# Kernel tuning notes

Hardware: AMD Instinct MI355X
Metric: run time of the kernel (lower is better)

## Reference

```python
import jax, jax.numpy as jnp
import numpy as np

B, P, S = 128, 10, 8
L, BF = 81, 75
OF, MF2 = 40, 20
C = 64
H = 3 * C  # hidden_size = 192
NCHAR = 8
EPS = 1e-5


def setup_inputs() -> dict:
    key = jax.random.key(0)
    ks = jax.random.split(key, 24)
    n = lambda i, shp: jax.random.normal(ks[i], shp, jnp.float32)
    w = lambda i, shp: jax.random.normal(ks[i], shp, jnp.float32) * 0.02
    return {
        "board": n(0, (B, P, S, L, BF)),
        "order": n(1, (B, P, S, OF)),
        "message": n(2, (B, P, S, MF2)),
        "other_ind": jax.random.uniform(ks[3], (B, P, 7), jnp.float32),
        "me_ind": jax.random.uniform(ks[4], (B, P, 7), jnp.float32),
        "h0": n(5, (P, B, H)),
        "c0": n(6, (P, B, H)),
        "Wb1": w(7, (1024, L * BF)), "bb1": jnp.zeros((1024,), jnp.float32),
        "Wb2": w(8, (256, 1024)), "bb2": jnp.zeros((256,), jnp.float32),
        "Wb3": w(9, (C, 256)), "bb3": jnp.zeros((C,), jnp.float32),
        "Wo1": w(10, (128, OF)), "bo1": jnp.zeros((128,), jnp.float32),
        "Wo2": w(11, (32, 128)), "bo2": jnp.zeros((32,), jnp.float32),
        "Wo3": w(12, (C, 32)), "bo3": jnp.zeros((C,), jnp.float32),
        "Wm1": w(13, (64, MF2)), "bm1": jnp.zeros((64,), jnp.float32),
        "Wm2": w(14, (32, 64)), "bm2": jnp.zeros((32,), jnp.float32),
        "Wm3": w(15, (C, 32)), "bm3": jnp.zeros((C,), jnp.float32),
        "g1": jnp.ones((C,), jnp.float32), "be1": jnp.zeros((C,), jnp.float32),
        "g2": jnp.ones((C,), jnp.float32), "be2": jnp.zeros((C,), jnp.float32),
        "g3": jnp.ones((C,), jnp.float32), "be3": jnp.zeros((C,), jnp.float32),
        "Wih": w(16, (4 * H, H)), "Whh": w(17, (4 * H, H)),
        "bih": jnp.zeros((4 * H,), jnp.float32), "bhh": jnp.zeros((4 * H,), jnp.float32),
        "Wf1": w(18, (256, S * H)), "bf1": jnp.zeros((256,), jnp.float32),
        "Wf2": w(19, (NCHAR, 256 + 14)), "bf2": jnp.zeros((NCHAR,), jnp.float32),
    }


def _mlp3(x, W1, b1, W2, b2, W3, b3):
    x = jax.nn.relu(x @ W1.T + b1)
    x = jax.nn.relu(x @ W2.T + b2)
    return x @ W3.T + b3


def _bn_relu(x, g, b):
    # x: [b, C, S]; BatchNorm1d in training mode -> biased batch stats over (N, L)
    m = x.mean(axis=(0, 2), keepdims=True)
    v = jnp.mean((x - m) ** 2, axis=(0, 2), keepdims=True)
    return jax.nn.relu(g[None, :, None] * (x - m) * jax.lax.rsqrt(v + EPS) + b[None, :, None])


def _forward(board, order, message, other_ind, me_ind, h0, c0,
             Wb1, bb1, Wb2, bb2, Wb3, bb3, Wo1, bo1, Wo2, bo2, Wo3, bo3,
             Wm1, bm1, Wm2, bm2, Wm3, bm3, g1, be1, g2, be2, g3, be3,
             Wih, Whh, bih, bhh, Wf1, bf1, Wf2, bf2):
    num_step = board.shape[2]

    def per_past(board_p, order_p, msg_p, oi_p, mi_p, h, c):
        bb = board_p.shape[0]
        bf = _mlp3(board_p.reshape(bb * num_step, -1), Wb1, bb1, Wb2, bb2, Wb3, bb3)
        bf = _bn_relu(jnp.swapaxes(bf.reshape(bb, num_step, -1), 1, 2), g1, be1)
        of = _mlp3(order_p.reshape(bb * num_step, -1), Wo1, bo1, Wo2, bo2, Wo3, bo3)
        of = _bn_relu(jnp.swapaxes(of.reshape(bb, num_step, -1), 1, 2), g2, be2)
        mf = _mlp3(msg_p.reshape(bb * num_step, -1), Wm1, bm1, Wm2, bm2, Wm3, bm3)
        mf = _bn_relu(jnp.swapaxes(mf.reshape(bb, num_step, -1), 1, 2), g3, be3)
        x_feat = jnp.concatenate([bf, of, mf], axis=-1)              # [b, C, 3S]
        x_feat = jnp.transpose(jnp.swapaxes(x_feat, 1, 2), (2, 0, 1))  # [C, b, 3S]
        x_feat = x_feat.reshape(num_step, bb, -1)                    # [S, b, H] (same C-order reindex as torch)

        def step(carry, xt):
            h_, c_ = carry
            gates = xt @ Wih.T + bih + h_ @ Whh.T + bhh
            i, f, g_, o = jnp.split(gates, 4, axis=-1)
            c_ = jax.nn.sigmoid(f) * c_ + jax.nn.sigmoid(i) * jnp.tanh(g_)
            h_ = jax.nn.sigmoid(o) * jnp.tanh(c_)
            return (h_, c_), h_

        _, outs = jax.lax.scan(step, (h, c), x_feat)  # [S, b, H]
        x = jnp.swapaxes(outs, 0, 1).reshape(bb, -1)  # [b, S*H]
        x = jax.nn.relu(x @ Wf1.T + bf1)
        x = jnp.concatenate([x, oi_p, mi_p], axis=-1)  # [b, 256+14]
        return x @ Wf2.T + bf2

    per = jax.vmap(per_past)(
        jnp.swapaxes(board, 0, 1), jnp.swapaxes(order, 0, 1), jnp.swapaxes(message, 0, 1),
        jnp.swapaxes(other_ind, 0, 1), jnp.swapaxes(me_ind, 0, 1), h0, c0)  # [P, b, NCHAR]
    return per.sum(axis=0)


def reference(board, order, message, other_ind, me_ind, h0, c0,
              Wb1, bb1, Wb2, bb2, Wb3, bb3, Wo1, bo1, Wo2, bo2, Wo3, bo3,
              Wm1, bm1, Wm2, bm2, Wm3, bm3, g1, be1, g2, be2, g3, be3,
              Wih, Whh, bih, bhh, Wf1, bf1, Wf2, bf2):
    return _forward(board, order, message, other_ind, me_ind, h0, c0,
                    Wb1, bb1, Wb2, bb2, Wb3, bb3, Wo1, bo1, Wo2, bo2, Wo3, bo3,
                    Wm1, bm1, Wm2, bm2, Wm3, bm3, g1, be1, g2, be2, g3, be3,
                    Wih, Whh, bih, bhh, Wf1, bf1, Wf2, bf2)
```

## Files before the change

### kernel.cpp

```cpp
#include <hip/hip_runtime.h>
#include <stdint.h>

typedef unsigned short u16;
typedef __bf16 v8bf __attribute__((ext_vector_type(8)));
typedef float  v4f  __attribute__((ext_vector_type(4)));

__device__ __forceinline__ u16 f2bf(float f) {
    union { float f; unsigned u; } x; x.f = f;
    unsigned r = (x.u + 0x7FFFu + ((x.u >> 16) & 1u)) >> 16;
    return (u16)r;
}
__device__ __forceinline__ float sigf(float x) { return 1.f / (1.f + __expf(-x)); }
__device__ __forceinline__ void gload(const u16* src, u16* ldst) {
    __builtin_amdgcn_global_load_lds((const __attribute__((address_space(1))) void*)src,
                                     (__attribute__((address_space(3))) void*)ldst, 16, 0, 0);
}

#define OFF_ABF    0UL
#define OFF_XINBF  0UL
#define OFF_XG     3932160UL
#define OFF_FC1    44728320UL
#define OFF_WB1    125829120UL
#define OFF_C1     138412032UL
#define OFF_WB2    159383552UL
#define OFF_WB3    165150720UL
#define OFF_BFE    165216256UL
#define OFF_OFE    167837696UL
#define OFF_MFE    170459136UL
#define OFF_WIH    173095936UL
#define OFF_WHH    173390848UL
#define OFF_WF1    173685760UL
#define OFF_BSUM   174472192UL

__global__ void __launch_bounds__(256) conv_board(const float* __restrict__ src, u16* __restrict__ dst)
{
    int bid = blockIdx.x;
    int row = bid / 6, chunk = bid - row * 6;
    int k0 = chunk * 1024 + threadIdx.x * 4;
    const float* s = src + (long)row * 6075 + k0;
    u16* d = dst + (long)row * 6144 + k0;
    if (k0 + 4 <= 6075) {
        float f0 = s[0], f1 = s[1], f2 = s[2], f3 = s[3];
        uint2 v;
        v.x = (unsigned)f2bf(f0) | ((unsigned)f2bf(f1) << 16);
        v.y = (unsigned)f2bf(f2) | ((unsigned)f2bf(f3) << 16);
        *(uint2*)d = v;
    } else {
#pragma unroll
        for (int z = 0; z < 4; ++z) {
            int k = k0 + z;
            d[z] = f2bf(k < 6075 ? s[z] : 0.f);
        }
    }
}

__global__ void __launch_bounds__(256) conv_weights(
    const float* __restrict__ Wb1, const float* __restrict__ Wb2, const float* __restrict__ Wb3,
    const float* __restrict__ Wih, const float* __restrict__ Whh, const float* __restrict__ Wf1,
    const float* __restrict__ bih, const float* __restrict__ bhh,
    u16* __restrict__ dWb1, u16* __restrict__ dWb2, u16* __restrict__ dWb3,
    u16* __restrict__ dWih, u16* __restrict__ dWhh, u16* __restrict__ dWf1,
    float* __restrict__ bsum)
{
    const long C0 = 6291456, C1 = 6553600, C2 = 6586368, C3 = 6733824,
               C4 = 6881280, C5 = 7274496, C6 = 7275264;
    for (long i = (long)blockIdx.x * 256 + threadIdx.x; i < C6; i += (long)gridDim.x * 256) {
        if (i < C0) {
            int r = (int)(i / 6144), k = (int)(i % 6144);
            dWb1[i] = f2bf(k < 6075 ? Wb1[(long)r * 6075 + k] : 0.f);
        } else if (i < C1) {
            long j = i - C0;
            dWb2[j] = f2bf(Wb2[j]);
        } else if (i < C2) {
            long j = i - C1;
            dWb3[j] = f2bf(j < 16384 ? Wb3[j] : 0.f);
        } else if (i < C3) {
            long j = i - C2;
            dWih[j] = f2bf(Wih[j]);
        } else if (i < C4) {
            long j = i - C3;
            dWhh[j] = f2bf(Whh[j]);
        } else if (i < C5) {
            long j = i - C4;
            dWf1[j] = f2bf(Wf1[j]);
        } else {
            long j = i - C5;
            bsum[j] = bih[j] + bhh[j];
        }
    }
}

#define G160_LDS 73728
__global__ void __launch_bounds__(256, 2)
gemm160(const u16* __restrict__ A, const u16* __restrict__ B,
        const float* __restrict__ bias, u16* __restrict__ C, int K)
{
    extern __shared__ __align__(16) u16 smem[];
    const int tid = threadIdx.x, wv = tid >> 6, lane = tid & 63;
    const int bid = blockIdx.x;
    const int k8 = bid & 7;
    const int j  = bid >> 3;
    const int rowt = k8 + (j >> 3) * 8;
    const int col  = j & 7;
    const long m0 = (long)rowt * 160;
    const long n0 = (long)col * 128;

    const int sr8 = lane >> 3;
    const int sslot = (lane & 7) ^ sr8;
    const u16* Ag = A + (m0 + wv * 8 + sr8) * (long)K + sslot * 8;
    const u16* Bg = B + (n0 + wv * 8 + sr8) * (long)K + sslot * 8;
    const int wr = wv >> 1, wc = wv & 1;
    const int wm = wr * 80, wn = wc * 64;
    const int fr = lane & 15, hi = lane >> 4, fx = fr & 7;

    const int nk = K >> 6;
    v4f acc[5][4] = {};

    auto STAGE = [&](int buf, int t) {
        const long k0 = (long)t * 64;
        const int ab = buf * 18432;
#pragma unroll
        for (int r = 0; r < 5; ++r)
            gload(Ag + (long)r * 32 * K + k0, smem + ab + r * 2048 + wv * 512);
#pragma unroll
        for (int r = 0; r < 4; ++r)
            gload(Bg + (long)r * 32 * K + k0, smem + ab + 10240 + r * 2048 + wv * 512);
    };
    auto LDA_ = [&](int buf, int ks, int i) -> v8bf {
        return *(const v8bf*)(smem + buf * 18432 + (wm + i * 16 + fr) * 64 + ((ks * 4 + hi) ^ fx) * 8);
    };
    auto LDB_ = [&](int buf, int ks, int j2) -> v8bf {
        return *(const v8bf*)(smem + buf * 18432 + 10240 + (wn + j2 * 16 + fr) * 64 + ((ks * 4 + hi) ^ fx) * 8);
    };

    STAGE(0, 0);
    STAGE(1, 1);
    for (int t = 0; t < nk; ++t) {
        const int buf = t & 1;
        if (t + 1 < nk) { asm volatile("s_waitcnt vmcnt(9)" ::: "memory"); }
        else            { asm volatile("s_waitcnt vmcnt(0)" ::: "memory"); }
        asm volatile("s_barrier" ::: "memory");
        __builtin_amdgcn_s_setprio(1);
        v8bf a0[5], a1[5], b0[4], b1[4];
#pragma unroll
        for (int j2 = 0; j2 < 4; ++j2) b0[j2] = LDB_(buf, 0, j2);
#pragma unroll
        for (int i = 0; i < 5; ++i) a0[i] = LDA_(buf, 0, i);
        __builtin_amdgcn_sched_barrier(0);
#pragma unroll
        for (int j2 = 0; j2 < 4; ++j2) b1[j2] = LDB_(buf, 1, j2);
#pragma unroll
        for (int i = 0; i < 5; ++i) a1[i] = LDA_(buf, 1, i);
#pragma unroll
        for (int i = 0; i < 5; ++i)
#pragma unroll
            for (int j2 = 0; j2 < 4; ++j2)
                acc[i][j2] = __builtin_amdgcn_mfma_f32_16x16x32_bf16(a0[i], b0[j2], acc[i][j2], 0, 0, 0);
        __builtin_amdgcn_sched_barrier(0);
        __builtin_amdgcn_s_setprio(0);
        asm volatile("s_waitcnt lgkmcnt(0)" ::: "memory");
        __builtin_amdgcn_sched_barrier(0);
        asm volatile("s_barrier" ::: "memory");
        if (t + 2 < nk) STAGE(buf, t + 2);
        __builtin_amdgcn_s_setprio(1);
#pragma unroll
        for (int i = 0; i < 5; ++i)
#pragma unroll
            for (int j2 = 0; j2 < 4; ++j2)
                acc[i][j2] = __builtin_amdgcn_mfma_f32_16x16x32_bf16(a1[i], b1[j2], acc[i][j2], 0, 0, 0);
        __builtin_amdgcn_s_setprio(0);
    }

#pragma unroll
    for (int i = 0; i < 5; ++i) {
        const long mr = m0 + wm + i * 16 + hi * 4;
#pragma unroll
        for (int j2 = 0; j2 < 4; ++j2) {
            const long n = n0 + wn + j2 * 16 + fr;
            float bv = bias[n];
#pragma unroll
            for (int r = 0; r < 4; ++r) {
                float v = fmaxf(acc[i][j2][r] + bv, 0.f);
                C[(mr + r) * 1024L + n] = f2bf(v);
            }
        }
    }
}

#define L23_LDS 81920
__global__ void __launch_bounds__(512, 1)
gemm_l23(const u16* __restrict__ A, const u16* __restrict__ B, const float* __restrict__ b2,
         const u16* __restrict__ W3, const float* __restrict__ b3, float* __restrict__ Out)
{
    extern __shared__ __align__(16) u16 smem[];
    const int tid = threadIdx.x, wv = tid >> 6, lane = tid & 63;
    const long m0 = (long)blockIdx.x * 64;
    const int sr8 = lane >> 3;
    const int sslot = (lane & 7) ^ sr8;
    const u16* Ag = A + (m0 + wv * 8 + sr8) * 1024L + sslot * 8;
    const u16* Bg = B + (wv * 8 + sr8) * 1024L + sslot * 8;
    const int wr = wv >> 2, wc = wv & 3;
    const int wm = wr * 32, wn = wc * 64;
    const int fr = lane & 15, hi = lane >> 4, fx = fr & 7;

    v4f acc[2][4] = {};

    auto STAGE = [&](int buf, int t) {
        const long k0 = (long)t * 64;
        const int ab = buf * 20480;
        gload(Ag + k0, smem + ab + wv * 512);
#pragma unroll
        for (int r = 0; r < 4; ++r)
            gload(Bg + (long)r * 64 * 1024 + k0, smem + ab + 4096 + r * 4096 + wv * 512);
    };
    auto COMPUTE = [&](int buf) {
#pragma unroll
        for (int ks = 0; ks < 2; ++ks) {
            const int sw = ((ks * 4 + hi) ^ fx) * 8;
            v8bf a[2], b[4];
#pragma unroll
            for (int i = 0; i < 2; ++i)
                a[i] = *(const v8bf*)(smem + buf * 20480 + (wm + i * 16 + fr) * 64 + sw);
#pragma unroll
            for (int j = 0; j < 4; ++j)
                b[j] = *(const v8bf*)(smem + buf * 20480 + 4096 + (wn + j * 16 + fr) * 64 + sw);
#pragma unroll
            for (int i = 0; i < 2; ++i)
#pragma unroll
                for (int j = 0; j < 4; ++j)
                    acc[i][j] = __builtin_amdgcn_mfma_f32_16x16x32_bf16(a[i], b[j], acc[i][j], 0, 0, 0);
        }
    };

    STAGE(0, 0);
    __syncthreads();
    int t = 1;
    while (true) {
        if (t < 16) STAGE(1, t);
        COMPUTE(0);
        if (t >= 16) break;
        __syncthreads();
        ++t;
        if (t < 16) STAGE(0, t);
        COMPUTE(1);
        if (t >= 16) break;
        __syncthreads();
        ++t;
    }
    __syncthreads();
    u16* C2s = smem;
#pragma unroll
    for (int i = 0; i < 2; ++i) {
        const int rrow = wm + i * 16 + hi * 4;
#pragma unroll
        for (int j = 0; j < 4; ++j) {
            const int ccol = wn + j * 16 + fr;
            float bv = b2[ccol];
#pragma unroll
            for (int r = 0; r < 4; ++r)
                C2s[(rrow + r) * 264 + ccol] = f2bf(fmaxf(acc[i][j][r] + bv, 0.f));
        }
    }
    __syncthreads();
    if (wv < 4) {
        v4f a3[4] = {};
#pragma unroll
        for (int kk = 0; kk < 8; ++kk) {
            v8bf af = *(const v8bf*)(&C2s[(wv * 16 + fr) * 264 + kk * 32 + hi * 8]);
#pragma unroll
            for (int j = 0; j < 4; ++j) {
                v8bf bfr = *(const v8bf*)(W3 + (j * 16 + fr) * 256 + kk * 32 + hi * 8);
                a3[j] = __builtin_amdgcn_mfma_f32_16x16x32_bf16(af, bfr, a3[j], 0, 0, 0);
            }
        }
#pragma unroll
        for (int j = 0; j < 4; ++j) {
            int n = j * 16 + fr;
            float bv = b3[n];
#pragma unroll
            for (int q = 0; q < 4; ++q)
                Out[(m0 + wv * 16 + hi * 4 + q) * 64 + n] = a3[j][q] + bv;
        }
    }
}

template<int OBF, int RELU, int BIAS>
__global__ void __launch_bounds__(256)
gemm_bt(const u16* __restrict__ A, const u16* __restrict__ B,
        const float* __restrict__ bias, void* __restrict__ Cv,
        int M, int N, int K, int ldc)
{
    __shared__ __align__(16) u16 As[2][128 * 64];
    __shared__ __align__(16) u16 Bs[2][128 * 64];
    const int tid = threadIdx.x;
    const int wv = tid >> 6, lane = tid & 63;
    const long m0 = (long)blockIdx.y * 128;
    const long n0 = (long)blockIdx.x * 128;
    const int srow  = wv * 8 + (lane >> 3);
    const int sslot = (lane & 7) ^ (lane >> 3);
    const u16* Ag = A + (m0 + srow) * (long)K + sslot * 8;
    const u16* Bg = B + (n0 + srow) * (long)K + sslot * 8;
    const int wm = (wv >> 1) * 64, wn = (wv & 1) * 64;
    const int fr = lane & 15, hi = lane >> 4;
    const int fx = fr & 7;

    v4f acc[4][4] = {};
    const int nk = K >> 6;

    auto STAGE = [&](int buf, int k0) {
#pragma unroll
        for (int r = 0; r < 4; ++r)
            gload(Ag + (long)r * 32 * K + k0, &As[buf][r * 2048 + wv * 512]);
#pragma unroll
        for (int r = 0; r < 4; ++r)
            gload(Bg + (long)r * 32 * K + k0, &Bs[buf][r * 2048 + wv * 512]);
    };
    auto COMPUTE = [&](int buf) {
#pragma unroll
        for (int ks = 0; ks < 2; ++ks) {
            v8bf a[4], b[4];
            const int sw = (((ks * 4 + hi) ^ fx)) * 8;
#pragma unroll
            for (int i = 0; i < 4; ++i)
                a[i] = *(const v8bf*)(&As[buf][(wm + i * 16 + fr) * 64 + sw]);
#pragma unroll
            for (int j = 0; j < 4; ++j)
                b[j] = *(const v8bf*)(&Bs[buf][(wn + j * 16 + fr) * 64 + sw]);
#pragma unroll
            for (int i = 0; i < 4; ++i)
#pragma unroll
                for (int j = 0; j < 4; ++j)
                    acc[i][j] = __builtin_amdgcn_mfma_f32_16x16x32_bf16(a[i], b[j], acc[i][j], 0, 0, 0);
        }
    };

    STAGE(0, 0);
    __syncthreads();
    int t = 1;
    while (true) {
        if (t < nk) STAGE(1, t * 64);
        COMPUTE(0);
        if (t >= nk) break;
        __syncthreads();
        ++t;
        if (t < nk) STAGE(0, t * 64);
        COMPUTE(1);
        if (t >= nk) break;
        __syncthreads();
        ++t;
    }

#pragma unroll
    for (int i = 0; i < 4; ++i) {
        const long mr = m0 + wm + i * 16 + hi * 4;
#pragma unroll
        for (int j = 0; j < 4; ++j) {
            const long n = n0 + wn + j * 16 + fr;
            if (n < N) {
                float bv = BIAS ? bias[n] : 0.f;
#pragma unroll
                for (int r = 0; r < 4; ++r) {
                    float v = acc[i][j][r] + bv;
                    if (RELU) v = fmaxf(v, 0.f);
                    if (OBF) ((u16*)Cv)[(mr + r) * (long)ldc + n] = f2bf(v);
                    else     ((float*)Cv)[(mr + r) * (long)ldc + n] = v;
                }
            }
        }
    }
}

template<int D0, int D1>
__device__ __forceinline__ void mlp3_body(
    float* sm, const float* __restrict__ X,
    const float* __restrict__ W1, const float* __restrict__ B1,
    const float* __restrict__ W2, const float* __restrict__ B2,
    const float* __restrict__ W3, const float* __restrict__ B3,
    float* __restrict__ Out, int blk)
{
    float* w1s = sm;
    float* w2s = w1s + D0 * D1;
    float* w3s = w2s + D1 * 32;
    float* b1s = w3s + 32 * 64;
    float* b2s = b1s + D1;
    float* b3s = b2s + 32;
    float* xs  = b3s + 64;
    float* h1  = xs + 32 * D0;
    float* h2  = h1 + 32 * D1;

    const int tid = threadIdx.x;
    const long row0 = (long)blk * 32;

    for (int i = tid; i < D0 * D1; i += 256) { int k = i / D1, n = i % D1; w1s[i] = W1[n * D0 + k]; }
    for (int i = tid; i < D1 * 32; i += 256) { int k = i / 32,  n = i % 32; w2s[i] = W2[n * D1 + k]; }
    for (int i = tid; i < 32 * 64; i += 256) { int k = i / 64,  n = i % 64; w3s[i] = W3[n * 32 + k]; }
    if (tid < D1) b1s[tid] = B1[tid];
    if (tid < 32) b2s[tid] = B2[tid];
    if (tid < 64) b3s[tid] = B3[tid];
    for (int i = tid; i < 32 * D0; i += 256) xs[i] = X[(row0 + i / D0) * D0 + i % D0];
    __syncthreads();

    const int wv = tid >> 6, lane = tid & 63;
    const int r0 = wv * 8;
    {
        constexpr int NL = D1 / 64;
        float acc[NL][8];
#pragma unroll
        for (int a = 0; a < NL; ++a)
#pragma unroll
            for (int r = 0; r < 8; ++r) acc[a][r] = 0.f;
        for (int k = 0; k < D0; ++k) {
            float w[NL];
#pragma unroll
            for (int a = 0; a < NL; ++a) w[a] = w1s[k * D1 + lane + a * 64];
#pragma unroll
            for (int r = 0; r < 8; ++r) {
                float x = xs[(r0 + r) * D0 + k];
#pragma unroll
                for (int a = 0; a < NL; ++a) acc[a][r] += w[a] * x;
            }
        }
#pragma unroll
        for (int a = 0; a < NL; ++a)
#pragma unroll
            for (int r = 0; r < 8; ++r)
                h1[(r0 + r) * D1 + lane + a * 64] = fmaxf(acc[a][r] + b1s[lane + a * 64], 0.f);
    }
    __syncthreads();
    {
        int n = lane & 31;
        int rb = r0 + (lane >> 5) * 4;
        float acc[4] = {0, 0, 0, 0};
        for (int k = 0; k < D1; ++k) {
            float w = w2s[k * 32 + n];
#pragma unroll
            for (int r = 0; r < 4; ++r) acc[r] += w * h1[(rb + r) * D1 + k];
        }
#pragma unroll
        for (int r = 0; r < 4; ++r) h2[(rb + r) * 32 + n] = fmaxf(acc[r] + b2s[n], 0.f);
    }
    __syncthreads();
    {
        float acc[8] = {};
        for (int k = 0; k < 32; ++k) {
            float w = w3s[k * 64 + lane];
#pragma unroll
            for (int r = 0; r < 8; ++r) acc[r] += w * h2[(r0 + r) * 32 + k];
        }
#pragma unroll
        for (int r = 0; r < 8; ++r) Out[(row0 + r0 + r) * 64 + lane] = acc[r] + b3s[lane];
    }
}

#define MLP_LDS 71552
__global__ void __launch_bounds__(256)
mlp3_dual(const float* __restrict__ Xo,
          const float* __restrict__ Wo1, const float* __restrict__ bo1,
          const float* __restrict__ Wo2, const float* __restrict__ bo2,
          const float* __restrict__ Wo3, const float* __restrict__ bo3,
          float* __restrict__ ofe,
          const float* __restrict__ Xm,
          const float* __restrict__ Wm1, const float* __restrict__ bm1,
          const float* __restrict__ Wm2, const float* __restrict__ bm2,
          const float* __restrict__ Wm3, const float* __restrict__ bm3,
          float* __restrict__ mfe)
{
    extern __shared__ __align__(16) float sm[];
    if (blockIdx.x < 320)
        mlp3_body<40, 128>(sm, Xo, Wo1, bo1, Wo2, bo2, Wo3, bo3, ofe, blockIdx.x);
    else
        mlp3_body<20, 64>(sm, Xm, Wm1, bm1, Wm2, bm2, Wm3, bm3, mfe, blockIdx.x - 320);
}

#define BX_LDS 100032
__global__ void __launch_bounds__(256, 1)
build_xin2(const float* __restrict__ bfe, const float* __restrict__ ofe, const float* __restrict__ mfe,
           const float* __restrict__ g1, const float* __restrict__ be1,
           const float* __restrict__ g2, const float* __restrict__ be2,
           const float* __restrict__ g3, const float* __restrict__ be3,
           u16* __restrict__ xin)
{
    extern __shared__ __align__(16) float ls[];
    float* coefA = ls + 24576;
    float* coefB = coefA + 24;
    float* psum  = coefB + 24;
    float* psum2 = psum + 192;
    const int p = blockIdx.x >> 3, s = blockIdx.x & 7;
    const int tid = threadIdx.x;
    const float* Fs[3] = {bfe, ofe, mfe};
    for (int g = tid; g < 3072; g += 256) {
        int br = g >> 10, rr = g & 1023, bb = rr >> 3, tt = rr & 7;
        const float* srcp = Fs[br] + ((long)(bb * 80 + p * 8 + tt)) * 64 + s * 8;
        float4 v0 = *(const float4*)srcp;
        float4 v1 = *(const float4*)(srcp + 4);
        *(float4*)(ls + (long)g * 8) = v0;
        *(float4*)(ls + (long)g * 8 + 4) = v1;
    }
    __syncthreads();
    if (tid < 192) {
        int pair = tid >> 3, part = tid & 7;
        int br = pair >> 3, cl = pair & 7;
        float s1 = 0.f, s2 = 0.f;
        for (int b2 = 0; b2 < 16; ++b2) {
            int bb = part * 16 + b2;
            const float* base = ls + ((br * 128 + bb) * 8) * 8 + cl;
#pragma unroll
            for (int tt = 0; tt < 8; ++tt) { float v = base[tt * 8]; s1 += v; s2 += v * v; }
        }
        psum[tid] = s1; psum2[tid] = s2;
    }
    __syncthreads();
    if (tid < 24) {
        float s1 = 0.f, s2 = 0.f;
#pragma unroll
        for (int q = 0; q < 8; ++q) { s1 += psum[tid * 8 + q]; s2 += psum2[tid * 8 + q]; }
        int br = tid >> 3, cl = tid & 7, c = s * 8 + cl;
        const float* G  = br == 0 ? g1  : (br == 1 ? g2  : g3);
        const float* BE = br == 0 ? be1 : (br == 1 ? be2 : be3);
        float m  = s1 * (1.f / 1024.f);
        float var = s2 * (1.f / 1024.f) - m * m;
        float Aa = G[c] * rsqrtf(var + 1e-5f);
        coefA[tid] = Aa;
        coefB[tid] = BE[c] - Aa * m;
    }
    __syncthreads();
    const int u = tid >> 1, h0 = (tid & 1) * 96;
    const long obase = ((long)(p * 8 + s) * 128 + u) * 192 + h0;
    const int cl = u >> 4;
    const int ub = (u & 15) * 8;
    union { u16 u[8]; uint4 v; } pk;
    for (int hq = 0; hq < 12; ++hq) {
#pragma unroll
        for (int z = 0; z < 8; ++z) {
            int h = h0 + hq * 8 + z;
            int bb = ub + h / 24, t = h % 24, br = t >> 3, tt = t & 7;
            float v = ls[((br * 128 + bb) * 8 + tt) * 8 + cl];
            float r = fmaxf(v * coefA[br * 8 + cl] + coefB[br * 8 + cl], 0.f);
            pk.u[z] = f2bf(r);
        }
        *(uint4*)(xin + obase + hq * 8) = pk.v;
    }
}

#define LSTM_LDS (6400 + 24576)
__global__ void __launch_bounds__(512, 1)
lstm_persist(const float* __restrict__ Xg, const u16* __restrict__ Whh,
             const float* __restrict__ h0, const float* __restrict__ c0,
             const u16* __restrict__ Wf1, const float* __restrict__ bf1,
             float* __restrict__ fc1o)
{
    extern __shared__ __align__(16) u16 smem[];
    u16*   hS    = smem;
    float* gates = (float*)(smem + 16 * 200);

    const int tid = threadIdx.x, wv = tid >> 6, lane = tid & 63;
    const int R0 = blockIdx.x * 8;
    const int fr = lane & 15, hi = lane >> 4;

    v8bf Wreg[6][6];
#pragma unroll
    for (int nt = 0; nt < 6; ++nt)
#pragma unroll
        for (int ks = 0; ks < 6; ++ks)
            Wreg[nt][ks] = *(const v8bf*)(Whh + (long)(nt * 128 + wv * 16 + fr) * 192 + ks * 32 + hi * 8);

    for (int i = tid; i < 16 * 200; i += 512) {
        int r = i / 200, cx = i % 200;
        u16 v = 0;
        if (r < 8 && cx < 192) v = f2bf(h0[(R0 + r) * 192 + cx]);
        hS[i] = v;
    }
    float creg[3];
#pragma unroll
    for (int j = 0; j < 3; ++j) {
        int e = j * 512 + tid;
        creg[j] = c0[(R0 + e / 192) * 192 + e % 192];
    }

    v4f f1acc[2] = {};
    const int nb0 = wv * 32;
    auto WF1ACC = [&](int ss, const v8bf* a) {
#pragma unroll
        for (int jf = 0; jf < 2; ++jf) {
            v4f tacc = f1acc[jf];
#pragma unroll
            for (int ks = 0; ks < 6; ++ks) {
                v8bf bfr = *(const v8bf*)(Wf1 + (long)(nb0 + jf * 16 + fr) * 1536 + ss * 192 + ks * 32 + hi * 8);
                tacc = __builtin_amdgcn_mfma_f32_16x16x32_bf16(a[ks], bfr, tacc, 0, 0, 0);
            }
            f1acc[jf] = tacc;
        }
    };

    for (int s = 0; s < 8; ++s) {
        __syncthreads();
        v8bf a[6];
#pragma unroll
        for (int ks = 0; ks < 6; ++ks)
            a[ks] = *(const v8bf*)(&hS[fr * 200 + ks * 32 + hi * 8]);
        if (s > 0) WF1ACC(s - 1, a);
#pragma unroll
        for (int nt = 0; nt < 6; ++nt) {
            v4f acc = {};
#pragma unroll
            for (int ks = 0; ks < 6; ++ks)
                acc = __builtin_amdgcn_mfma_f32_16x16x32_bf16(a[ks], Wreg[nt][ks], acc, 0, 0, 0);
            int n = nt * 128 + wv * 16 + fr;
            if (hi < 2) {
#pragma unroll
                for (int q = 0; q < 4; ++q)
                    gates[(hi * 4 + q) * 768 + n] = acc[q];
            }
        }
        __syncthreads();
#pragma unroll
        for (int j = 0; j < 3; ++j) {
            int e = j * 512 + tid;
            int r = e / 192, hd = e % 192;
            int grow = R0 + r;
            int p = grow >> 7, u = grow & 127;
            long xrow = (long)((p * 8 + s) * 128 + u) * 768;
            float gi = Xg[xrow + hd]       + gates[r * 768 + hd];
            float gf = Xg[xrow + 192 + hd] + gates[r * 768 + 192 + hd];
            float gg = Xg[xrow + 384 + hd] + gates[r * 768 + 384 + hd];
            float go = Xg[xrow + 576 + hd] + gates[r * 768 + 576 + hd];
            float c = sigf(gf) * creg[j] + sigf(gi) * tanhf(gg);
            float h = sigf(go) * tanhf(c);
            creg[j] = c;
            hS[r * 200 + hd] = f2bf(h);
        }
    }
    __syncthreads();
    {
        v8bf a[6];
#pragma unroll
        for (int ks = 0; ks < 6; ++ks)
            a[ks] = *(const v8bf*)(&hS[fr * 200 + ks * 32 + hi * 8]);
        WF1ACC(7, a);
    }
    if (hi < 2) {
#pragma unroll
        for (int jf = 0; jf < 2; ++jf)
#pragma unroll
            for (int q = 0; q < 4; ++q) {
                int row = hi * 4 + q;
                int n = nb0 + jf * 16 + fr;
                fc1o[(long)(R0 + row) * 256 + n] = fmaxf(f1acc[jf][q] + bf1[n], 0.f);
            }
    }
}

__global__ void __launch_bounds__(256) final_fc2(
    const float* __restrict__ fc1, const float* __restrict__ oi, const float* __restrict__ mi,
    const float* __restrict__ Wf2, const float* __restrict__ bf2, float* __restrict__ out)
{
    const int wv = threadIdx.x >> 6, lane = threadIdx.x & 63;
    const int w = blockIdx.x * 4 + wv;
    const int u = w >> 3, n = w & 7;
    const float* wrow = Wf2 + n * 270;
    float wreg[4];
#pragma unroll
    for (int q = 0; q < 4; ++q) wreg[q] = wrow[lane + 64 * q];
    float wtail = (lane < 14) ? wrow[256 + lane] : 0.f;
    float acc = 0.f;
    for (int p = 0; p < 10; ++p) {
        const float* x = fc1 + (long)(p * 128 + u) * 256;
#pragma unroll
        for (int q = 0; q < 4; ++q) acc += x[lane + 64 * q] * wreg[q];
        float t = 0.f;
        if (lane < 7)       t = oi[(u * 10 + p) * 7 + lane];
        else if (lane < 14) t = mi[(u * 10 + p) * 7 + lane - 7];
        acc += t * wtail;
    }
#pragma unroll
    for (int off = 32; off; off >>= 1) acc += __shfl_xor(acc, off);
    if (lane == 0) out[u * 8 + n] = acc + bf2[n];
}

extern "C" void kernel_launch(void* const* d_in, const int* in_sizes, int n_in,
                              void* d_out, int out_size, void* d_ws, size_t ws_size,
                              hipStream_t stream)
{
    (void)in_sizes; (void)n_in; (void)out_size; (void)ws_size;
    const float* board = (const float*)d_in[0];
    const float* order = (const float*)d_in[1];
    const float* mess  = (const float*)d_in[2];
    const float* oi    = (const float*)d_in[3];
    const float* mi    = (const float*)d_in[4];
    const float* h0    = (const float*)d_in[5];
    const float* c0    = (const float*)d_in[6];
    const float* Wb1 = (const float*)d_in[7];  const float* bb1 = (const float*)d_in[8];
    const float* Wb2 = (const float*)d_in[9];  const float* bb2 = (const float*)d_in[10];
    const float* Wb3 = (const float*)d_in[11]; const float* bb3 = (const float*)d_in[12];
    const float* Wo1 = (const float*)d_in[13]; const float* bo1 = (const float*)d_in[14];
    const float* Wo2 = (const float*)d_in[15]; const float* bo2 = (const float*)d_in[16];
    const float* Wo3 = (const float*)d_in[17]; const float* bo3 = (const float*)d_in[18];
    const float* Wm1 = (const float*)d_in[19]; const float* bm1 = (const float*)d_in[20];
    const float* Wm2 = (const float*)d_in[21]; const float* bm2 = (const float*)d_in[22];
    const float* Wm3 = (const float*)d_in[23]; const float* bm3 = (const float*)d_in[24];
    const float* g1  = (const float*)d_in[25]; const float* be1 = (const float*)d_in[26];
    const float* g2  = (const float*)d_in[27]; const float* be2 = (const float*)d_in[28];
    const float* g3  = (const float*)d_in[29]; const float* be3 = (const float*)d_in[30];
    const float* Wih = (const float*)d_in[31]; const float* Whh = (const float*)d_in[32];
    const float* bih = (const float*)d_in[33]; const float* bhh = (const float*)d_in[34];
    const float* Wf1 = (const float*)d_in[35]; const float* bf1 = (const float*)d_in[36];
    const float* Wf2 = (const float*)d_in[37]; const float* bf2 = (const float*)d_in[38];

    uint8_t* ws = (uint8_t*)d_ws;
    u16*   A_bf    = (u16*)(ws + OFF_ABF);
    u16*   xin_bf  = (u16*)(ws + OFF_XINBF);
    float* Xg      = (float*)(ws + OFF_XG);
    float* fc1o    = (float*)(ws + OFF_FC1);
    u16*   Wb1_bf  = (u16*)(ws + OFF_WB1);
    u16*   C1_bf   = (u16*)(ws + OFF_C1);
    u16*   Wb2_bf  = (u16*)(ws + OFF_WB2);
    u16*   Wb3_bf  = (u16*)(ws + OFF_WB3);
    float* bfe     = (float*)(ws + OFF_BFE);
    float* ofe     = (float*)(ws + OFF_OFE);
    float* mfe     = (float*)(ws + OFF_MFE);
    u16*   Wih_bf  = (u16*)(ws + OFF_WIH);
    u16*   Whh_bf  = (u16*)(ws + OFF_WHH);
    u16*   Wf1_bf  = (u16*)(ws + OFF_WF1);
    float* bsum    = (float*)(ws + OFF_BSUM);

    conv_board<<<61440, 256, 0, stream>>>(board, A_bf);
    conv_weights<<<2048, 256, 0, stream>>>(Wb1, Wb2, Wb3, Wih, Whh, Wf1, bih, bhh,
                                           Wb1_bf, Wb2_bf, Wb3_bf, Wih_bf, Whh_bf, Wf1_bf, bsum);

    hipFuncSetAttribute(reinterpret_cast<const void*>(gemm160),
                        hipFuncAttributeMaxDynamicSharedMemorySize, G160_LDS);
    gemm160<<<512, 256, G160_LDS, stream>>>(A_bf, Wb1_bf, bb1, C1_bf, 6144);
    hipFuncSetAttribute(reinterpret_cast<const void*>(gemm_l23),
                        hipFuncAttributeMaxDynamicSharedMemorySize, L23_LDS);
    gemm_l23<<<160, 512, L23_LDS, stream>>>(C1_bf, Wb2_bf, bb2, Wb3_bf, bb3, bfe);

    hipFuncSetAttribute(reinterpret_cast<const void*>(mlp3_dual),
                        hipFuncAttributeMaxDynamicSharedMemorySize, MLP_LDS);
    mlp3_dual<<<640, 256, MLP_LDS, stream>>>(order, Wo1, bo1, Wo2, bo2, Wo3, bo3, ofe,
                                             mess, Wm1, bm1, Wm2, bm2, Wm3, bm3, mfe);

    hipFuncSetAttribute(reinterpret_cast<const void*>(build_xin2),
                        hipFuncAttributeMaxDynamicSharedMemorySize, BX_LDS);
    build_xin2<<<80, 256, BX_LDS, stream>>>(bfe, ofe, mfe, g1, be1, g2, be2, g3, be3, xin_bf);

    gemm_bt<0, 0, 1><<<dim3(6, 80), 256, 0, stream>>>(xin_bf, Wih_bf, bsum, Xg, 10240, 768, 192, 768);

    hipFuncSetAttribute(reinterpret_cast<const void*>(lstm_persist),
                        hipFuncAttributeMaxDynamicSharedMemorySize, LSTM_LDS);
    lstm_persist<<<160, 512, LSTM_LDS, stream>>>(Xg, Whh_bf, h0, c0, Wf1_bf, bf1, fc1o);

    final_fc2<<<256, 256, 0, stream>>>(fc1o, oi, mi, Wf2, bf2, (float*)d_out);
}
```

Baseline: 354.4 us.

## Fuse LSTM input projection into BN build kernel and merge prep kernels

The batch-norm/ReLU input builder now keeps its bf16 LSTM input tile in swizzled LDS and computes the Wih projection with MFMA directly, writing Xg. This removes the separate gemm_bt launch and the global round trip of xin. The two conversion kernels (board and weights) are also merged into one launch. The tradeoff is that the fused projection runs on only 80 blocks with 1 block per CU, each doing a 128x768x192 GEMM, which may underuse the GPU compared with the 480-block gemm_bt.

```diff
diff --git a/kernel.cpp b/kernel.cpp
--- a/kernel.cpp
+++ b/kernel.cpp
@@ -17,7 +17,6 @@
 }
 
 #define OFF_ABF    0UL
-#define OFF_XINBF  0UL
 #define OFF_XG     3932160UL
 #define OFF_FC1    44728320UL
 #define OFF_WB1    125829120UL
@@ -32,29 +31,8 @@
 #define OFF_WF1    173685760UL
 #define OFF_BSUM   174472192UL
 
-__global__ void __launch_bounds__(256) conv_board(const float* __restrict__ src, u16* __restrict__ dst)
-{
-    int bid = blockIdx.x;
-    int row = bid / 6, chunk = bid - row * 6;
-    int k0 = chunk * 1024 + threadIdx.x * 4;
-    const float* s = src + (long)row * 6075 + k0;
-    u16* d = dst + (long)row * 6144 + k0;
-    if (k0 + 4 <= 6075) {
-        float f0 = s[0], f1 = s[1], f2 = s[2], f3 = s[3];
-        uint2 v;
-        v.x = (unsigned)f2bf(f0) | ((unsigned)f2bf(f1) << 16);
-        v.y = (unsigned)f2bf(f2) | ((unsigned)f2bf(f3) << 16);
-        *(uint2*)d = v;
-    } else {
-#pragma unroll
-        for (int z = 0; z < 4; ++z) {
-            int k = k0 + z;
-            d[z] = f2bf(k < 6075 ? s[z] : 0.f);
-        }
-    }
-}
-
-__global__ void __launch_bounds__(256) conv_weights(
+__global__ void __launch_bounds__(256) prep(
+    const float* __restrict__ board, u16* __restrict__ A_bf,
     const float* __restrict__ Wb1, const float* __restrict__ Wb2, const float* __restrict__ Wb3,
     const float* __restrict__ Wih, const float* __restrict__ Whh, const float* __restrict__ Wf1,
     const float* __restrict__ bih, const float* __restrict__ bhh,
@@ -62,9 +40,30 @@
     u16* __restrict__ dWih, u16* __restrict__ dWhh, u16* __restrict__ dWf1,
     float* __restrict__ bsum)
 {
+    int bid = blockIdx.x;
+    if (bid < 61440) {
+        int row = bid / 6, chunk = bid - row * 6;
+        int k0 = chunk * 1024 + threadIdx.x * 4;
+        const float* s = board + (long)row * 6075 + k0;
+        u16* d = A_bf + (long)row * 6144 + k0;
+        if (k0 + 4 <= 6075) {
+            float f0 = s[0], f1 = s[1], f2 = s[2], f3 = s[3];
+            uint2 v;
+            v.x = (unsigned)f2bf(f0) | ((unsigned)f2bf(f1) << 16);
+            v.y = (unsigned)f2bf(f2) | ((unsigned)f2bf(f3) << 16);
+            *(uint2*)d = v;
+        } else {
+#pragma unroll
+            for (int z = 0; z < 4; ++z) {
+                int k = k0 + z;
+                d[z] = f2bf(k < 6075 ? s[z] : 0.f);
+            }
+        }
+        return;
+    }
     const long C0 = 6291456, C1 = 6553600, C2 = 6586368, C3 = 6733824,
                C4 = 6881280, C5 = 7274496, C6 = 7275264;
-    for (long i = (long)blockIdx.x * 256 + threadIdx.x; i < C6; i += (long)gridDim.x * 256) {
+    for (long i = (long)(bid - 61440) * 256 + threadIdx.x; i < C6; i += 2048L * 256) {
         if (i < C0) {
             int r = (int)(i / 6144), k = (int)(i % 6144);
             dWb1[i] = f2bf(k < 6075 ? Wb1[(long)r * 6075 + k] : 0.f);
@@ -284,92 +283,6 @@
     }
 }
 
-template<int OBF, int RELU, int BIAS>
-__global__ void __launch_bounds__(256)
-gemm_bt(const u16* __restrict__ A, const u16* __restrict__ B,
-        const float* __restrict__ bias, void* __restrict__ Cv,
-        int M, int N, int K, int ldc)
-{
-    __shared__ __align__(16) u16 As[2][128 * 64];
-    __shared__ __align__(16) u16 Bs[2][128 * 64];
-    const int tid = threadIdx.x;
-    const int wv = tid >> 6, lane = tid & 63;
-    const long m0 = (long)blockIdx.y * 128;
-    const long n0 = (long)blockIdx.x * 128;
-    const int srow  = wv * 8 + (lane >> 3);
-    const int sslot = (lane & 7) ^ (lane >> 3);
-    const u16* Ag = A + (m0 + srow) * (long)K + sslot * 8;
-    const u16* Bg = B + (n0 + srow) * (long)K + sslot * 8;
-    const int wm = (wv >> 1) * 64, wn = (wv & 1) * 64;
-    const int fr = lane & 15, hi = lane >> 4;
-    const int fx = fr & 7;
-
-    v4f acc[4][4] = {};
-    const int nk = K >> 6;
-
-    auto STAGE = [&](int buf, int k0) {
-#pragma unroll
-        for (int r = 0; r < 4; ++r)
-            gload(Ag + (long)r * 32 * K + k0, &As[buf][r * 2048 + wv * 512]);
-#pragma unroll
-        for (int r = 0; r < 4; ++r)
-            gload(Bg + (long)r * 32 * K + k0, &Bs[buf][r * 2048 + wv * 512]);
-    };
-    auto COMPUTE = [&](int buf) {
-#pragma unroll
-        for (int ks = 0; ks < 2; ++ks) {
-            v8bf a[4], b[4];
-            const int sw = (((ks * 4 + hi) ^ fx)) * 8;
-#pragma unroll
-            for (int i = 0; i < 4; ++i)
-                a[i] = *(const v8bf*)(&As[buf][(wm + i * 16 + fr) * 64 + sw]);
-#pragma unroll
-            for (int j = 0; j < 4; ++j)
-                b[j] = *(const v8bf*)(&Bs[buf][(wn + j * 16 + fr) * 64 + sw]);
-#pragma unroll
-            for (int i = 0; i < 4; ++i)
-#pragma unroll
-                for (int j = 0; j < 4; ++j)
-                    acc[i][j] = __builtin_amdgcn_mfma_f32_16x16x32_bf16(a[i], b[j], acc[i][j], 0, 0, 0);
-        }
-    };
-
-    STAGE(0, 0);
-    __syncthreads();
-    int t = 1;
-    while (true) {
-        if (t < nk) STAGE(1, t * 64);
-        COMPUTE(0);
-        if (t >= nk) break;
-        __syncthreads();
-        ++t;
-        if (t < nk) STAGE(0, t * 64);
-        COMPUTE(1);
-        if (t >= nk) break;
-        __syncthreads();
-        ++t;
-    }
-
-#pragma unroll
-    for (int i = 0; i < 4; ++i) {
-        const long mr = m0 + wm + i * 16 + hi * 4;
-#pragma unroll
-        for (int j = 0; j < 4; ++j) {
-            const long n = n0 + wn + j * 16 + fr;
-            if (n < N) {
-                float bv = BIAS ? bias[n] : 0.f;
-#pragma unroll
-                for (int r = 0; r < 4; ++r) {
-                    float v = acc[i][j][r] + bv;
-                    if (RELU) v = fmaxf(v, 0.f);
-                    if (OBF) ((u16*)Cv)[(mr + r) * (long)ldc + n] = f2bf(v);
-                    else     ((float*)Cv)[(mr + r) * (long)ldc + n] = v;
-                }
-            }
-        }
-    }
-}
-
 template<int D0, int D1>
 __device__ __forceinline__ void mlp3_body(
     float* sm, const float* __restrict__ X,
@@ -472,19 +385,21 @@
         mlp3_body<20, 64>(sm, Xm, Wm1, bm1, Wm2, bm2, Wm3, bm3, mfe, blockIdx.x - 320);
 }
 
-#define BX_LDS 100032
+#define BXG_LDS 149504
 __global__ void __launch_bounds__(256, 1)
-build_xin2(const float* __restrict__ bfe, const float* __restrict__ ofe, const float* __restrict__ mfe,
-           const float* __restrict__ g1, const float* __restrict__ be1,
-           const float* __restrict__ g2, const float* __restrict__ be2,
-           const float* __restrict__ g3, const float* __restrict__ be3,
-           u16* __restrict__ xin)
+build_xg(const float* __restrict__ bfe, const float* __restrict__ ofe, const float* __restrict__ mfe,
+         const float* __restrict__ g1, const float* __restrict__ be1,
+         const float* __restrict__ g2, const float* __restrict__ be2,
+         const float* __restrict__ g3, const float* __restrict__ be3,
+         const u16* __restrict__ Wih, const float* __restrict__ bsum,
+         float* __restrict__ Xg)
 {
     extern __shared__ __align__(16) float ls[];
     float* coefA = ls + 24576;
     float* coefB = coefA + 24;
     float* psum  = coefB + 24;
     float* psum2 = psum + 192;
+    u16* xs16 = (u16*)((char*)ls + 100352);
     const int p = blockIdx.x >> 3, s = blockIdx.x & 7;
     const int tid = threadIdx.x;
     const float* Fs[3] = {bfe, ofe, mfe};
@@ -524,21 +439,49 @@
         coefB[tid] = BE[c] - Aa * m;
     }
     __syncthreads();
-    const int u = tid >> 1, h0 = (tid & 1) * 96;
-    const long obase = ((long)(p * 8 + s) * 128 + u) * 192 + h0;
-    const int cl = u >> 4;
-    const int ub = (u & 15) * 8;
-    union { u16 u[8]; uint4 v; } pk;
-    for (int hq = 0; hq < 12; ++hq) {
-#pragma unroll
-        for (int z = 0; z < 8; ++z) {
-            int h = h0 + hq * 8 + z;
-            int bb = ub + h / 24, t = h % 24, br = t >> 3, tt = t & 7;
-            float v = ls[((br * 128 + bb) * 8 + tt) * 8 + cl];
-            float r = fmaxf(v * coefA[br * 8 + cl] + coefB[br * 8 + cl], 0.f);
-            pk.u[z] = f2bf(r);
-        }
-        *(uint4*)(xin + obase + hq * 8) = pk.v;
+    {
+        const int u = tid >> 1, h0 = (tid & 1) * 96;
+        const int cl = u >> 4;
+        const int ub = (u & 15) * 8;
+        const int swr = u & 7;
+        union { u16 u[8]; uint4 v; } pk;
+        for (int hq = 0; hq < 12; ++hq) {
+#pragma unroll
+            for (int z = 0; z < 8; ++z) {
+                int h = h0 + hq * 8 + z;
+                int bb = ub + h / 24, t = h % 24, br = t >> 3, tt = t & 7;
+                float v = ls[((br * 128 + bb) * 8 + tt) * 8 + cl];
+                float r = fmaxf(v * coefA[br * 8 + cl] + coefB[br * 8 + cl], 0.f);
+                pk.u[z] = f2bf(r);
+            }
+            int slot = (tid & 1) * 12 + hq;
+            *(uint4*)(xs16 + u * 192 + ((slot ^ swr) * 8)) = pk.v;
+        }
+    }
+    __syncthreads();
+    const int wv = tid >> 6, lane = tid & 63;
+    const int fr = lane & 15, hi = lane >> 4;
+    const long R0 = (long)blockIdx.x * 128;
+    for (int nf = 0; nf < 12; ++nf) {
+        const int n = wv * 192 + nf * 16 + fr;
+        v8bf w[6];
+#pragma unroll
+        for (int k = 0; k < 6; ++k)
+            w[k] = *(const v8bf*)(Wih + (long)n * 192 + k * 32 + hi * 8);
+        float bv = bsum[n];
+#pragma unroll
+        for (int mf = 0; mf < 8; ++mf) {
+            const int r = mf * 16 + fr;
+            v4f acc = {};
+#pragma unroll
+            for (int k = 0; k < 6; ++k) {
+                v8bf a = *(const v8bf*)(xs16 + r * 192 + (((k * 4 + hi) ^ (r & 7)) * 8));
+                acc = __builtin_amdgcn_mfma_f32_16x16x32_bf16(a, w[k], acc, 0, 0, 0);
+            }
+#pragma unroll
+            for (int q = 0; q < 4; ++q)
+                Xg[(R0 + mf * 16 + hi * 4 + q) * 768 + n] = acc[q] + bv;
+        }
     }
 }
 
@@ -708,7 +651,6 @@
 
     uint8_t* ws = (uint8_t*)d_ws;
     u16*   A_bf    = (u16*)(ws + OFF_ABF);
-    u16*   xin_bf  = (u16*)(ws + OFF_XINBF);
     float* Xg      = (float*)(ws + OFF_XG);
     float* fc1o    = (float*)(ws + OFF_FC1);
     u16*   Wb1_bf  = (u16*)(ws + OFF_WB1);
@@ -723,9 +665,8 @@
     u16*   Wf1_bf  = (u16*)(ws + OFF_WF1);
     float* bsum    = (float*)(ws + OFF_BSUM);
 
-    conv_board<<<61440, 256, 0, stream>>>(board, A_bf);
-    conv_weights<<<2048, 256, 0, stream>>>(Wb1, Wb2, Wb3, Wih, Whh, Wf1, bih, bhh,
-                                           Wb1_bf, Wb2_bf, Wb3_bf, Wih_bf, Whh_bf, Wf1_bf, bsum);
+    prep<<<63488, 256, 0, stream>>>(board, A_bf, Wb1, Wb2, Wb3, Wih, Whh, Wf1, bih, bhh,
+                                    Wb1_bf, Wb2_bf, Wb3_bf, Wih_bf, Whh_bf, Wf1_bf, bsum);
 
     hipFuncSetAttribute(reinterpret_cast<const void*>(gemm160),
                         hipFuncAttributeMaxDynamicSharedMemorySize, G160_LDS);
@@ -739,11 +680,10 @@
     mlp3_dual<<<640, 256, MLP_LDS, stream>>>(order, Wo1, bo1, Wo2, bo2, Wo3, bo3, ofe,
                                              mess, Wm1, bm1, Wm2, bm2, Wm3, bm3, mfe);
 
-    hipFuncSetAttribute(reinterpret_cast<const void*>(build_xin2),
-                        hipFuncAttributeMaxDynamicSharedMemorySize, BX_LDS);
-    build_xin2<<<80, 256, BX_LDS, stream>>>(bfe, ofe, mfe, g1, be1, g2, be2, g3, be3, xin_bf);
-
-    gemm_bt<0, 0, 1><<<dim3(6, 80), 256, 0, stream>>>(xin_bf, Wih_bf, bsum, Xg, 10240, 768, 192, 768);
+    hipFuncSetAttribute(reinterpret_cast<const void*>(build_xg),
+                        hipFuncAttributeMaxDynamicSharedMemorySize, BXG_LDS);
+    build_xg<<<80, 256, BXG_LDS, stream>>>(bfe, ofe, mfe, g1, be1, g2, be2, g3, be3,
+                                           Wih_bf, bsum, Xg);
 
     hipFuncSetAttribute(reinterpret_cast<const void*>(lstm_persist),
                         hipFuncAttributeMaxDynamicSharedMemorySize, LSTM_LDS);
```

Result: no change. 347.9 us (-1.8%).
